# Optimization experiments

Hardware: AMD Instinct MI355X
Metric: run time of the kernel (lower is better)

Reference implementation:

```python
import jax, jax.numpy as jnp
import numpy as np

# BoxCoder weights and clamp from the torch module
WX, WY, WW, WH = 10.0, 10.0, 5.0, 5.0
BBOX_CLIP = float(np.log(1000.0 / 16.0))
SCORE_THRESH = 0.05
NMS_THRESH = 0.5
DET_PER_IMG = 100
MIN_SIZE = 0.01
B, N, C = 4, 4096, 91
IMG_H, IMG_W = 800, 1216


def setup_inputs() -> dict:
    key = jax.random.key(0)
    k1, k2, k3, k4, k5, k6 = jax.random.split(key, 6)
    class_logits = jax.random.normal(k1, (B * N, C), dtype=jnp.float32) * 2.0
    box_regression = jax.random.normal(k2, (B * N, C * 4), dtype=jnp.float32) * 0.5
    # valid xyxy proposals inside the image
    x1 = jax.random.uniform(k3, (B, N)) * (0.7 * IMG_W)
    y1 = jax.random.uniform(k4, (B, N)) * (0.7 * IMG_H)
    bw = jax.random.uniform(k5, (B, N)) * (0.25 * IMG_W) + 4.0
    bh = jax.random.uniform(k6, (B, N)) * (0.25 * IMG_H) + 4.0
    proposals = jnp.stack([x1, y1, x1 + bw, y1 + bh], axis=-1)
    image_shapes = jnp.tile(jnp.array([[IMG_H, IMG_W]], dtype=jnp.int32), (B, 1))
    return {"class_logits": class_logits, "box_regression": box_regression,
            "proposals": proposals, "image_shapes": image_shapes}


def decode_boxes(deltas, proposals):
    # deltas [N, C, 4], proposals [N, 4] xyxy -> pred boxes [N, C, 4]
    w = proposals[:, 2] - proposals[:, 0]
    h = proposals[:, 3] - proposals[:, 1]
    cx = proposals[:, 0] + 0.5 * w
    cy = proposals[:, 1] + 0.5 * h
    dx = deltas[..., 0] / WX
    dy = deltas[..., 1] / WY
    dw = jnp.minimum(deltas[..., 2] / WW, BBOX_CLIP)
    dh = jnp.minimum(deltas[..., 3] / WH, BBOX_CLIP)
    pcx = dx * w[:, None] + cx[:, None]
    pcy = dy * h[:, None] + cy[:, None]
    pw = jnp.exp(dw) * w[:, None]
    ph = jnp.exp(dh) * h[:, None]
    return jnp.stack([pcx - 0.5 * pw, pcy - 0.5 * ph,
                      pcx + 0.5 * pw, pcy + 0.5 * ph], axis=-1)


def iou_one_many(box, boxes):
    # box [4] vs boxes [M, 4]
    lt = jnp.maximum(box[:2], boxes[:, :2])
    rb = jnp.minimum(box[2:], boxes[:, 2:])
    wh = jnp.clip(rb - lt, 0.0)
    inter = wh[:, 0] * wh[:, 1]
    a1 = (box[2] - box[0]) * (box[3] - box[1])
    a2 = (boxes[:, 2] - boxes[:, 0]) * (boxes[:, 3] - boxes[:, 1])
    return inter / (a1 + a2 - inter)


def nms_keep(off_boxes, live):
    # greedy NMS on class-offset boxes; selection is non-differentiable
    off_boxes = jax.lax.stop_gradient(off_boxes)
    live = jax.lax.stop_gradient(live)

    def body(lv, _):
        i = jnp.argmax(lv)
        s = lv[i]
        iou = iou_one_many(off_boxes[i], off_boxes)
        lv = jnp.where(iou > NMS_THRESH, -jnp.inf, lv)
        lv = lv.at[i].set(-jnp.inf)
        return lv, (i, jnp.isfinite(s))

    _, (keep, kvalid) = jax.lax.scan(body, live, None, length=DET_PER_IMG)
    return keep, kvalid  # [DET_PER_IMG] each


def postprocess_one(logits, deltas, proposals, hw):
    # logits [N, C], deltas [N, C*4], proposals [N, 4], hw [2] float (H, W)
    num_classes = logits.shape[-1]
    boxes = decode_boxes(deltas.reshape(-1, num_classes, 4), proposals)  # [N, C, 4]
    Hh, Ww = hw[0], hw[1]
    boxes = jnp.stack([jnp.clip(boxes[..., 0], 0.0, Ww),
                       jnp.clip(boxes[..., 1], 0.0, Hh),
                       jnp.clip(boxes[..., 2], 0.0, Ww),
                       jnp.clip(boxes[..., 3], 0.0, Hh)], axis=-1)
    scores = jax.nn.softmax(logits, axis=-1)
    labels = jnp.broadcast_to(jnp.arange(num_classes, dtype=jnp.int32), scores.shape)
    # drop background class 0, flatten per-class candidates -> M = N*(C-1)
    boxes = boxes[:, 1:].reshape(-1, 4)
    scores = scores[:, 1:].reshape(-1)
    labels = labels[:, 1:].reshape(-1)
    ws = boxes[:, 2] - boxes[:, 0]
    hs = boxes[:, 3] - boxes[:, 1]
    valid = (scores > SCORE_THRESH) & (ws >= MIN_SIZE) & (hs >= MIN_SIZE)
    # batched_nms: per-class coordinate offset so classes never overlap
    max_coord = jnp.max(boxes)
    off_boxes = boxes + (labels.astype(boxes.dtype) * (max_coord + 1.0))[:, None]
    live = jnp.where(valid, scores, -jnp.inf)
    keep, kvalid = nms_keep(off_boxes, live)
    out_boxes = jnp.where(kvalid[:, None], boxes[keep], 0.0)
    out_scores = jnp.where(kvalid, scores[keep], 0.0)
    out_labels = jnp.where(kvalid, labels[keep], -1)
    return out_boxes, out_scores, out_labels


def reference(class_logits, box_regression, proposals, image_shapes):
    b, n, _ = proposals.shape
    num_classes = class_logits.shape[-1]
    logits = class_logits.reshape(b, n, num_classes)
    deltas = box_regression.reshape(b, n, num_classes * 4)
    hw = image_shapes.astype(logits.dtype)
    boxes, scores, labels = jax.vmap(postprocess_one)(logits, deltas, proposals, hw)
    return boxes, scores, labels
```

## Files before the change

kernel.cpp:

```cpp
#include <hip/hip_runtime.h>
#include <math.h>
#include <float.h>
#include <limits.h>

#define NBATCH 4
#define NPROP  4096
#define NCLS   91
#define NFG    90
#define NDET   100
#define CCAP   1024
#define BN     (NBATCH * NPROP)
#define SLOTS  (NFG * NDET)
#define FCAP   16384
#define CHUNK  128
#define NWORD  128

static __device__ __forceinline__ float clampf(float x, float lo, float hi) {
    return fminf(fmaxf(x, lo), hi);
}

static __device__ __forceinline__ void decode_box(int b, int np, int c,
    const float* __restrict__ props, const float* __restrict__ deltas,
    float W, float H, float& bx1, float& by1, float& bx2, float& by2)
{
    const float* pr = props + ((size_t)b * NPROP + np) * 4;
    const float x1 = pr[0], y1 = pr[1], x2 = pr[2], y2 = pr[3];
    const float w = x2 - x1, h = y2 - y1;
    const float cx = x1 + 0.5f * w, cy = y1 + 0.5f * h;
    const float* d = deltas + (((size_t)b * NPROP + np) * NCLS + c) * 4;
    const float BBC = 4.135166556742356f;
    const float dx = d[0] / 10.0f;
    const float dy = d[1] / 10.0f;
    const float dw = fminf(d[2] / 5.0f, BBC);
    const float dh = fminf(d[3] / 5.0f, BBC);
    const float pcx = dx * w + cx;
    const float pcy = dy * h + cy;
    const float pw = expf(dw) * w;
    const float ph = expf(dh) * h;
    bx1 = clampf(pcx - 0.5f * pw, 0.0f, W);
    by1 = clampf(pcy - 0.5f * ph, 0.0f, H);
    bx2 = clampf(pcx + 0.5f * pw, 0.0f, W);
    by2 = clampf(pcy + 0.5f * ph, 0.0f, H);
}

static __device__ __forceinline__ bool iou_gt(const float4 S, const float4 Q, float aq)
{
    const float iw = fmaxf(fminf(S.z, Q.z) - fmaxf(S.x, Q.x), 0.0f);
    const float ih = fmaxf(fminf(S.w, Q.w) - fmaxf(S.y, Q.y), 0.0f);
    const float inter = iw * ih;
    const float as = (S.z - S.x) * (S.w - S.y);
    return inter / (as + aq - inter) > 0.5f;
}

static __device__ __forceinline__ int block_excl_scan(int v, int t, int* wtot)
{
    const int lane = t & 63, wid = t >> 6;
    int inc = v;
    #pragma unroll
    for (int s = 1; s < 64; s <<= 1) {
        const int u = __shfl_up(inc, s);
        if (lane >= s) inc += u;
    }
    if (lane == 63) wtot[wid] = inc;
    __syncthreads();
    int base = 0;
    for (int w2 = 0; w2 < wid; ++w2) base += wtot[w2];
    __syncthreads();
    return base + inc - v;
}

__global__ __launch_bounds__(256) void stats_mask_kernel(
    const float* __restrict__ logits, const float* __restrict__ props,
    const float* __restrict__ deltas, const int* __restrict__ imgsh,
    float2* __restrict__ stats, unsigned* __restrict__ mask)
{
    const int wavei = threadIdx.x >> 6;
    const int lane  = threadIdx.x & 63;
    const int p = blockIdx.x * 4 + wavei;
    const int b = p >> 12;
    const int np = p & (NPROP - 1);
    const float* lrow = logits + (size_t)p * NCLS;

    const float a  = lrow[lane];
    const float a2 = (lane + 64 < NCLS) ? lrow[lane + 64] : -INFINITY;

    float m = fmaxf(a, a2);
    #pragma unroll
    for (int s = 32; s > 0; s >>= 1) m = fmaxf(m, __shfl_down(m, s));
    m = __shfl(m, 0);

    const float e0 = expf(a - m);
    const float e1 = (lane + 64 < NCLS) ? expf(a2 - m) : 0.0f;
    float sum = e0 + e1;
    #pragma unroll
    for (int s = 32; s > 0; s >>= 1) sum += __shfl_down(sum, s);
    sum = __shfl(sum, 0);

    const float W = (float)imgsh[b * 2 + 1];
    const float H = (float)imgsh[b * 2 + 0];

    bool pass0 = ((e0 / sum) > 0.05f) && (lane >= 1);
    if (pass0) {
        float bx1, by1, bx2, by2;
        decode_box(b, np, lane, props, deltas, W, H, bx1, by1, bx2, by2);
        pass0 = ((bx2 - bx1) >= 0.01f) && ((by2 - by1) >= 0.01f);
    }
    bool pass1 = ((e1 / sum) > 0.05f);
    if (pass1) {
        float bx1, by1, bx2, by2;
        decode_box(b, np, lane + 64, props, deltas, W, H, bx1, by1, bx2, by2);
        pass1 = ((bx2 - bx1) >= 0.01f) && ((by2 - by1) >= 0.01f);
    }

    const unsigned long long b0 = __ballot(pass0);
    const unsigned long long b1 = __ballot(pass1);

    if (lane == 0) {
        stats[p] = make_float2(m, sum);
        mask[p]          = (unsigned)b0;
        mask[BN + p]     = (unsigned)(b0 >> 32);
        mask[2 * BN + p] = (unsigned)b1;
    }
}

__global__ __launch_bounds__(256) void maskt_kernel(
    const unsigned* __restrict__ mask, unsigned* __restrict__ maskT)
{
    const int blk = blockIdx.x;
    const int b = blk >> 4;
    const int s = blk & 15;
    const int t = threadIdx.x;
    __shared__ unsigned lm[3 * 256];

    #pragma unroll
    for (int j = 0; j < 3; ++j)
        lm[j * 256 + t] = mask[(size_t)j * BN + b * NPROP + s * 256 + t];
    __syncthreads();

    for (int idx = t; idx < NCLS * 8; idx += 256) {
        const int c = idx >> 3, w = idx & 7;
        const int plane = c >> 5, bitpos = c & 31;
        const unsigned* src = &lm[plane * 256 + w * 32];
        unsigned word = 0;
        #pragma unroll
        for (int k = 0; k < 32; ++k)
            word |= ((src[k] >> bitpos) & 1u) << k;
        maskT[((size_t)(b * NCLS + c)) * NWORD + s * 8 + w] = word;
    }
}

__global__ __launch_bounds__(256) void class_nms_kernel(
    const float* __restrict__ logits, const float2* __restrict__ stats,
    const unsigned* __restrict__ maskT,
    const float* __restrict__ props, const float* __restrict__ deltas,
    const int* __restrict__ imgsh, unsigned long long* __restrict__ svKeys)
{
    const int blk  = blockIdx.x;
    const int b    = blk / NFG;
    const int cm1  = blk % NFG;
    const int c    = cm1 + 1;
    const int t    = threadIdx.x;
    const int lane = t & 63;

    __shared__ unsigned wbuf[NWORD];
    __shared__ int wt2[2];
    __shared__ unsigned long long sk[CCAP];
    __shared__ unsigned long long sks[CCAP];
    __shared__ float4 sbox[CCAP];
    __shared__ unsigned long long mrow[CHUNK][2];
    __shared__ float4 sOwn[NDET];
    __shared__ unsigned long long sPreW[2];
    __shared__ int s_ns;

    const unsigned* col = maskT + ((size_t)(b * NCLS + c)) * NWORD;
    if (t < NWORD) wbuf[t] = col[t];
    __syncthreads();

    const int pc = (t < NWORD) ? __popc(wbuf[t]) : 0;
    int inc = pc;
    #pragma unroll
    for (int s = 1; s < 64; s <<= 1) {
        const int u = __shfl_up(inc, s);
        if (lane >= s) inc += u;
    }
    if (lane == 63 && (t >> 6) < 2) wt2[t >> 6] = inc;
    __syncthreads();
    const int ntot = wt2[0] + wt2[1];
    const int n = min(ntot, CCAP);
    if (n == 0) {
        for (int i = t; i < NDET; i += 256) svKeys[(size_t)blk * NDET + i] = 0ULL;
        return;
    }
    const int myoff = ((t >> 6) == 1 ? wt2[0] : 0) + inc - pc;

    if (t < NWORD) {
        unsigned wv = wbuf[t];
        int o = myoff;
        while (wv) {
            const int k = __ffs(wv) - 1; wv &= wv - 1;
            const int np = t * 32 + k;
            const int p = b * NPROP + np;
            const float lg = logits[(size_t)p * NCLS + c];
            const float2 st = stats[p];
            const float score = expf(lg - st.x) / st.y;
            const unsigned flat = (unsigned)(np * NFG + cm1);
            const unsigned long long key =
                ((unsigned long long)__float_as_uint(score) << 32) | (unsigned)(~flat);
            if (o < CCAP) sk[o] = key;
            ++o;
        }
    }
    __syncthreads();

    {
        unsigned long long myk[4];
        int rnk[4] = {0, 0, 0, 0};
        #pragma unroll
        for (int e = 0; e < 4; ++e)
            myk[e] = (t + e * 256 < n) ? sk[t + e * 256] : 0ULL;
        #pragma unroll 4
        for (int j = 0; j < n; ++j) {
            const unsigned long long kj = sk[j];
            #pragma unroll
            for (int e = 0; e < 4; ++e) rnk[e] += (kj > myk[e]) ? 1 : 0;
        }
        #pragma unroll
        for (int e = 0; e < 4; ++e)
            if (t + e * 256 < n) sks[rnk[e]] = myk[e];
    }
    __syncthreads();

    const float W = (float)imgsh[b * 2 + 1];
    const float H = (float)imgsh[b * 2 + 0];
    for (int i = t; i < n; i += 256) {
        const unsigned flat = ~(unsigned)sks[i];
        const int np = flat / NFG;
        float bx1, by1, bx2, by2;
        decode_box(b, np, c, props, deltas, W, H, bx1, by1, bx2, by2);
        sbox[i] = make_float4(bx1, by1, bx2, by2);
    }
    if (t == 0) s_ns = 0;
    __syncthreads();

    int nsTot = 0;
    for (int cb = 0; cb < n && nsTot < NDET; cb += CHUNK) {
        const int C = min(CHUNK, n - cb);

        bool pre = false;
        if (t < C) {
            const float4 Q = sbox[cb + t];
            const float aq = (Q.z - Q.x) * (Q.w - Q.y);
            for (int l = 0; l < nsTot; ++l) {
                if (iou_gt(sOwn[l], Q, aq)) { pre = true; break; }
            }
        }
        const unsigned long long bal = __ballot(pre);
        if (t == 0)  sPreW[0] = bal;
        if (t == 64) sPreW[1] = bal;

        {
            const int r = t >> 1, w = t & 1;
            unsigned long long word = 0ULL;
            if (r < C) {
                const float4 R = sbox[cb + r];
                const int j0 = w * 64;
                const int jend = min(j0 + 64, C);
                for (int j = (j0 > r + 1 ? j0 : r + 1); j < jend; ++j) {
                    const float4 Q = sbox[cb + j];
                    const float aq = (Q.z - Q.x) * (Q.w - Q.y);
                    if (iou_gt(R, Q, aq)) word |= (1ULL << (j - j0));
                }
            }
            mrow[r][w] = word;
        }
        __syncthreads();

        if (t == 0) {
            unsigned long long S0 = sPreW[0], S1 = sPreW[1];
            int ns = nsTot;
            unsigned long long r0 = mrow[0][0], r1 = mrow[0][1];
            for (int i = 0; i < C && ns < NDET; ++i) {
                const unsigned long long nr0 = (i + 1 < C) ? mrow[i + 1][0] : 0ULL;
                const unsigned long long nr1 = (i + 1 < C) ? mrow[i + 1][1] : 0ULL;
                const bool dead = (i < 64) ? ((S0 >> i) & 1ULL)
                                           : ((S1 >> (i - 64)) & 1ULL);
                if (!dead) {
                    sOwn[ns] = sbox[cb + i];
                    svKeys[(size_t)blk * NDET + ns] = sks[cb + i];
                    ++ns;
                    S0 |= r0; S1 |= r1;
                }
                r0 = nr0; r1 = nr1;
            }
            s_ns = ns;
        }
        __syncthreads();
        nsTot = s_ns;
    }

    for (int i = nsTot + t; i < NDET; i += 256) svKeys[(size_t)blk * NDET + i] = 0ULL;
}

__global__ __launch_bounds__(1024) void select_kernel(
    const unsigned long long* __restrict__ svKeys,
    const float* __restrict__ props, const float* __restrict__ deltas,
    const int* __restrict__ imgsh, float* __restrict__ out)
{
    const int b = blockIdx.x;
    const int t = threadIdx.x;
    __shared__ unsigned long long F[FCAP];
    __shared__ int hist[4096];
    __shared__ int wtot[16];
    __shared__ int s_T, s_above, s_total;

    if (t == 0) { s_T = -1; s_above = 0; s_total = 0; }
    #pragma unroll
    for (int j = 0; j < 4; ++j) hist[t + j * 1024] = 0;

    const unsigned long long* src = svKeys + (size_t)b * SLOTS;
    unsigned long long keys[9];
    #pragma unroll
    for (int j = 0; j < 9; ++j) {
        const int s = t + j * 1024;
        keys[j] = (s < SLOTS) ? src[s] : 0ULL;
    }
    __syncthreads();

    #pragma unroll
    for (int j = 0; j < 9; ++j) {
        if (keys[j] != 0ULL) atomicAdd(&hist[(unsigned)(keys[j] >> 52)], 1);
    }
    __syncthreads();

    {
        const int gbase = (1023 - t) * 4;
        const int s0 = hist[gbase] + hist[gbase + 1] + hist[gbase + 2] + hist[gbase + 3];
        const int pre = block_excl_scan(s0, t, wtot);
        int acc = pre;
        for (int d = gbase + 3; d >= gbase; --d) {
            const int h = hist[d];
            if (acc < NDET && acc + h >= NDET) { s_T = d; s_above = acc; }
            acc += h;
        }
        if (t == 1023) s_total = acc;
    }
    __syncthreads();

    const int T = s_T;
    const int total = s_total;
    const int n2 = (T < 0) ? total : (s_above + hist[T]);
    const bool fast = (n2 <= 2048);

    int mycnt = 0;
    #pragma unroll
    for (int j = 0; j < 9; ++j) {
        const unsigned long long k = keys[j];
        const bool m = (k != 0ULL) && (fast ? (T < 0 || (int)(k >> 52) >= T) : true);
        mycnt += m ? 1 : 0;
    }
    int off = block_excl_scan(mycnt, t, wtot);
    #pragma unroll
    for (int j = 0; j < 9; ++j) {
        const unsigned long long k = keys[j];
        const bool m = (k != 0ULL) && (fast ? (T < 0 || (int)(k >> 52) >= T) : true);
        if (m) F[off++] = k;
    }
    const int nsort = fast ? n2 : total;

    int P = 128; while (P < nsort) P <<= 1;
    for (int i = nsort + t; i < P; i += 1024) F[i] = 0ULL;

    for (unsigned kk = 2; kk <= (unsigned)P; kk <<= 1) {
        for (unsigned jj = kk >> 1; jj > 0; jj >>= 1) {
            __syncthreads();
            for (unsigned i = t; i < (unsigned)P; i += 1024) {
                const unsigned ixj = i ^ jj;
                if (ixj > i) {
                    const unsigned long long x = F[i], y = F[ixj];
                    const bool up = ((i & kk) == 0);
                    if (up ? (x < y) : (x > y)) { F[i] = y; F[ixj] = x; }
                }
            }
        }
    }
    __syncthreads();

    float* oB = out + (size_t)b * NDET * 4;
    float* oS = out + (size_t)NBATCH * NDET * 4 + (size_t)b * NDET;
    float* oL = out + (size_t)NBATCH * NDET * 5 + (size_t)b * NDET;
    if (t < NDET) {
        const unsigned long long key = F[t];
        if (key != 0ULL) {
            const unsigned flat = ~(unsigned)key;
            const float score = __uint_as_float((unsigned)(key >> 32));
            const int np = flat / NFG;
            const int c  = (int)(flat - (unsigned)np * NFG) + 1;
            const float W = (float)imgsh[b * 2 + 1];
            const float H = (float)imgsh[b * 2 + 0];
            float bx1, by1, bx2, by2;
            decode_box(b, np, c, props, deltas, W, H, bx1, by1, bx2, by2);
            oB[t * 4 + 0] = bx1; oB[t * 4 + 1] = by1;
            oB[t * 4 + 2] = bx2; oB[t * 4 + 3] = by2;
            oS[t] = score;
            oL[t] = (float)c;
        } else {
            oB[t * 4 + 0] = 0.0f; oB[t * 4 + 1] = 0.0f;
            oB[t * 4 + 2] = 0.0f; oB[t * 4 + 3] = 0.0f;
            oS[t] = 0.0f; oL[t] = -1.0f;
        }
    }
}

extern "C" void kernel_launch(void* const* d_in, const int* in_sizes, int n_in,
                              void* d_out, int out_size, void* d_ws, size_t ws_size,
                              hipStream_t stream)
{
    const float* logits = (const float*)d_in[0];
    const float* deltas = (const float*)d_in[1];
    const float* props  = (const float*)d_in[2];
    const int*   imgsh  = (const int*)d_in[3];
    float* out = (float*)d_out;

    char* w = (char*)d_ws;
    float2* stats = (float2*)w;            w += (size_t)BN * sizeof(float2);
    unsigned* mask = (unsigned*)w;         w += (size_t)3 * BN * sizeof(unsigned);
    unsigned long long* svKeys = (unsigned long long*)w;
    w += (size_t)NBATCH * SLOTS * sizeof(unsigned long long);
    unsigned* maskT = (unsigned*)w;
    w += (size_t)NBATCH * NCLS * NWORD * sizeof(unsigned);

    stats_mask_kernel<<<BN / 4, 256, 0, stream>>>(logits, props, deltas, imgsh, stats, mask);
    maskt_kernel<<<NBATCH * 16, 256, 0, stream>>>(mask, maskT);
    class_nms_kernel<<<NBATCH * NFG, 256, 0, stream>>>(
        logits, stats, maskT, props, deltas, imgsh, svKeys);
    select_kernel<<<NBATCH, 1024, 0, stream>>>(svKeys, props, deltas, imgsh, out);
}
```

Measured before the change: 74.73 us.

## Precompute candidate keys and decoded boxes in parallel per-proposal expand kernel

```diff
diff --git a/kernel.cpp b/kernel.cpp
--- a/kernel.cpp
+++ b/kernel.cpp
@@ -149,75 +149,115 @@
     }
 }
 
+__global__ __launch_bounds__(128) void offsets_kernel(
+    const unsigned* __restrict__ maskT, int* __restrict__ wordOff, int* __restrict__ cnt)
+{
+    const int blk = blockIdx.x;
+    const int b   = blk / NFG;
+    const int c   = blk % NFG + 1;
+    const int t   = threadIdx.x;
+    const int lane = t & 63;
+    __shared__ int wt2[2];
+
+    const unsigned w = maskT[((size_t)(b * NCLS + c)) * NWORD + t];
+    const int pc = __popc(w);
+    int inc = pc;
+    #pragma unroll
+    for (int s = 1; s < 64; s <<= 1) {
+        const int u = __shfl_up(inc, s);
+        if (lane >= s) inc += u;
+    }
+    if (lane == 63) wt2[t >> 6] = inc;
+    __syncthreads();
+    const int myoff = ((t >> 6) == 1 ? wt2[0] : 0) + inc - pc;
+    wordOff[(size_t)blk * NWORD + t] = myoff;
+    if (t == 127) cnt[blk] = wt2[0] + wt2[1];
+}
+
+__global__ __launch_bounds__(256) void expand_kernel(
+    const float* __restrict__ logits, const float2* __restrict__ stats,
+    const unsigned* __restrict__ mask, const unsigned* __restrict__ maskT,
+    const int* __restrict__ wordOff,
+    const float* __restrict__ props, const float* __restrict__ deltas,
+    const int* __restrict__ imgsh,
+    unsigned long long* __restrict__ cKeys, float4* __restrict__ cBox)
+{
+    const int wavei = threadIdx.x >> 6;
+    const int lane  = threadIdx.x & 63;
+    const int p = blockIdx.x * 4 + wavei;
+    const int b = p >> 12;
+    const int np = p & (NPROP - 1);
+
+    const unsigned m0 = mask[p];
+    const unsigned m1 = mask[BN + p];
+    const unsigned m2 = mask[2 * BN + p];
+    if (!(m0 | m1 | m2)) return;
+
+    const float2 st = stats[p];
+    const float* lrow = logits + (size_t)p * NCLS;
+    const float W = (float)imgsh[b * 2 + 1];
+    const float H = (float)imgsh[b * 2 + 0];
+    const int wrd = np >> 5;
+    const unsigned below = (1u << (np & 31)) - 1u;
+
+    #pragma unroll
+    for (int half = 0; half < 2; ++half) {
+        const int c = lane + half * 64;
+        if (c < 1 || c >= NCLS) continue;
+        const unsigned plane = (half == 0) ? ((c < 32) ? m0 : m1) : m2;
+        if (!((plane >> (c & 31)) & 1u)) continue;
+        const int cm1 = c - 1;
+        const float score = expf(lrow[c] - st.x) / st.y;
+        const unsigned flat = (unsigned)(np * NFG + cm1);
+        const unsigned long long key =
+            ((unsigned long long)__float_as_uint(score) << 32) | (unsigned)(~flat);
+        float bx1, by1, bx2, by2;
+        decode_box(b, np, c, props, deltas, W, H, bx1, by1, bx2, by2);
+        const unsigned mtw = maskT[((size_t)(b * NCLS + c)) * NWORD + wrd];
+        const int bucket = b * NFG + cm1;
+        const int pos = wordOff[(size_t)bucket * NWORD + wrd] + __popc(mtw & below);
+        if (pos < CCAP) {
+            cKeys[(size_t)bucket * CCAP + pos] = key;
+            cBox[(size_t)bucket * CCAP + pos]  = make_float4(bx1, by1, bx2, by2);
+        }
+    }
+}
+
 __global__ __launch_bounds__(256) void class_nms_kernel(
-    const float* __restrict__ logits, const float2* __restrict__ stats,
-    const unsigned* __restrict__ maskT,
-    const float* __restrict__ props, const float* __restrict__ deltas,
-    const int* __restrict__ imgsh, unsigned long long* __restrict__ svKeys)
+    const int* __restrict__ cnt, const unsigned long long* __restrict__ cKeys,
+    const float4* __restrict__ cBox, unsigned long long* __restrict__ svKeys)
 {
     const int blk  = blockIdx.x;
-    const int b    = blk / NFG;
-    const int cm1  = blk % NFG;
-    const int c    = cm1 + 1;
     const int t    = threadIdx.x;
-    const int lane = t & 63;
-
-    __shared__ unsigned wbuf[NWORD];
-    __shared__ int wt2[2];
+
     __shared__ unsigned long long sk[CCAP];
     __shared__ unsigned long long sks[CCAP];
-    __shared__ float4 sbox[CCAP];
+    __shared__ float4 sboxS[CCAP];
     __shared__ unsigned long long mrow[CHUNK][2];
     __shared__ float4 sOwn[NDET];
     __shared__ unsigned long long sPreW[2];
     __shared__ int s_ns;
 
-    const unsigned* col = maskT + ((size_t)(b * NCLS + c)) * NWORD;
-    if (t < NWORD) wbuf[t] = col[t];
-    __syncthreads();
-
-    const int pc = (t < NWORD) ? __popc(wbuf[t]) : 0;
-    int inc = pc;
-    #pragma unroll
-    for (int s = 1; s < 64; s <<= 1) {
-        const int u = __shfl_up(inc, s);
-        if (lane >= s) inc += u;
-    }
-    if (lane == 63 && (t >> 6) < 2) wt2[t >> 6] = inc;
-    __syncthreads();
-    const int ntot = wt2[0] + wt2[1];
-    const int n = min(ntot, CCAP);
+    const int n = min(cnt[blk], CCAP);
     if (n == 0) {
         for (int i = t; i < NDET; i += 256) svKeys[(size_t)blk * NDET + i] = 0ULL;
         return;
     }
-    const int myoff = ((t >> 6) == 1 ? wt2[0] : 0) + inc - pc;
-
-    if (t < NWORD) {
-        unsigned wv = wbuf[t];
-        int o = myoff;
-        while (wv) {
-            const int k = __ffs(wv) - 1; wv &= wv - 1;
-            const int np = t * 32 + k;
-            const int p = b * NPROP + np;
-            const float lg = logits[(size_t)p * NCLS + c];
-            const float2 st = stats[p];
-            const float score = expf(lg - st.x) / st.y;
-            const unsigned flat = (unsigned)(np * NFG + cm1);
-            const unsigned long long key =
-                ((unsigned long long)__float_as_uint(score) << 32) | (unsigned)(~flat);
-            if (o < CCAP) sk[o] = key;
-            ++o;
-        }
-    }
+    const unsigned long long* srcK = cKeys + (size_t)blk * CCAP;
+    const float4* srcB = cBox + (size_t)blk * CCAP;
+    for (int i = t; i < n; i += 256) sk[i] = srcK[i];
     __syncthreads();
 
     {
         unsigned long long myk[4];
+        float4 myb[4];
         int rnk[4] = {0, 0, 0, 0};
         #pragma unroll
-        for (int e = 0; e < 4; ++e)
-            myk[e] = (t + e * 256 < n) ? sk[t + e * 256] : 0ULL;
+        for (int e = 0; e < 4; ++e) {
+            const int i = t + e * 256;
+            myk[e] = (i < n) ? sk[i] : 0ULL;
+            myb[e] = (i < n) ? srcB[i] : make_float4(0.f, 0.f, 0.f, 0.f);
+        }
         #pragma unroll 4
         for (int j = 0; j < n; ++j) {
             const unsigned long long kj = sk[j];
@@ -225,19 +265,9 @@
             for (int e = 0; e < 4; ++e) rnk[e] += (kj > myk[e]) ? 1 : 0;
         }
         #pragma unroll
-        for (int e = 0; e < 4; ++e)
-            if (t + e * 256 < n) sks[rnk[e]] = myk[e];
-    }
-    __syncthreads();
-
-    const float W = (float)imgsh[b * 2 + 1];
-    const float H = (float)imgsh[b * 2 + 0];
-    for (int i = t; i < n; i += 256) {
-        const unsigned flat = ~(unsigned)sks[i];
-        const int np = flat / NFG;
-        float bx1, by1, bx2, by2;
-        decode_box(b, np, c, props, deltas, W, H, bx1, by1, bx2, by2);
-        sbox[i] = make_float4(bx1, by1, bx2, by2);
+        for (int e = 0; e < 4; ++e) {
+            if (t + e * 256 < n) { sks[rnk[e]] = myk[e]; sboxS[rnk[e]] = myb[e]; }
+        }
     }
     if (t == 0) s_ns = 0;
     __syncthreads();
@@ -248,7 +278,7 @@
 
         bool pre = false;
         if (t < C) {
-            const float4 Q = sbox[cb + t];
+            const float4 Q = sboxS[cb + t];
             const float aq = (Q.z - Q.x) * (Q.w - Q.y);
             for (int l = 0; l < nsTot; ++l) {
                 if (iou_gt(sOwn[l], Q, aq)) { pre = true; break; }
@@ -262,11 +292,11 @@
             const int r = t >> 1, w = t & 1;
             unsigned long long word = 0ULL;
             if (r < C) {
-                const float4 R = sbox[cb + r];
+                const float4 R = sboxS[cb + r];
                 const int j0 = w * 64;
                 const int jend = min(j0 + 64, C);
                 for (int j = (j0 > r + 1 ? j0 : r + 1); j < jend; ++j) {
-                    const float4 Q = sbox[cb + j];
+                    const float4 Q = sboxS[cb + j];
                     const float aq = (Q.z - Q.x) * (Q.w - Q.y);
                     if (iou_gt(R, Q, aq)) word |= (1ULL << (j - j0));
                 }
@@ -285,7 +315,7 @@
                 const bool dead = (i < 64) ? ((S0 >> i) & 1ULL)
                                            : ((S1 >> (i - 64)) & 1ULL);
                 if (!dead) {
-                    sOwn[ns] = sbox[cb + i];
+                    sOwn[ns] = sboxS[cb + i];
                     svKeys[(size_t)blk * NDET + ns] = sks[cb + i];
                     ++ns;
                     S0 |= r0; S1 |= r1;
@@ -428,10 +458,18 @@
     w += (size_t)NBATCH * SLOTS * sizeof(unsigned long long);
     unsigned* maskT = (unsigned*)w;
     w += (size_t)NBATCH * NCLS * NWORD * sizeof(unsigned);
+    int* wordOff = (int*)w;                w += (size_t)NBATCH * NFG * NWORD * sizeof(int);
+    int* cnt = (int*)w;                    w += 4096;
+    unsigned long long* cKeys = (unsigned long long*)w;
+    w += (size_t)NBATCH * NFG * CCAP * sizeof(unsigned long long);
+    float4* cBox = (float4*)w;
+    w += (size_t)NBATCH * NFG * CCAP * sizeof(float4);
 
     stats_mask_kernel<<<BN / 4, 256, 0, stream>>>(logits, props, deltas, imgsh, stats, mask);
     maskt_kernel<<<NBATCH * 16, 256, 0, stream>>>(mask, maskT);
-    class_nms_kernel<<<NBATCH * NFG, 256, 0, stream>>>(
-        logits, stats, maskT, props, deltas, imgsh, svKeys);
+    offsets_kernel<<<NBATCH * NFG, 128, 0, stream>>>(maskT, wordOff, cnt);
+    expand_kernel<<<BN / 4, 256, 0, stream>>>(
+        logits, stats, mask, maskT, wordOff, props, deltas, imgsh, cKeys, cBox);
+    class_nms_kernel<<<NBATCH * NFG, 256, 0, stream>>>(cnt, cKeys, cBox, svKeys);
     select_kernel<<<NBATCH, 1024, 0, stream>>>(svKeys, props, deltas, imgsh, out);
 }
```

Result: slower. 83.68 us (+12.0%).
